# Optimization experiments

Hardware: AMD Instinct MI355X
Metric: run time of the kernel (lower is better)

Reference implementation:

```python
import jax, jax.numpy as jnp
import numpy as np

COMMITMENT_COST = 1.0


def setup_inputs() -> dict:
    key = jax.random.key(0)
    k1, k2 = jax.random.split(key)
    x = jax.random.normal(k1, (8, 4096, 256), dtype=jnp.float32)
    codebook = jax.random.normal(k2, (2048, 256), dtype=jnp.float32)
    return {"x": x, "codebook": codebook}


def reference(x, codebook):
    # Squared Euclidean distances via the GEMM expansion:
    # argmin over torch.cdist (sqrt is monotone); dist values are unused.
    x2 = jnp.sum(x * x, axis=-1, keepdims=True)            # [B, T, 1]
    c2 = jnp.sum(codebook * codebook, axis=-1)             # [N]
    d2 = x2 - 2.0 * jnp.einsum('btd,nd->btn', x, codebook) + c2  # [B, T, N]
    indices = jnp.argmin(d2, axis=-1)                      # [B, T]
    codes = codebook[indices]                              # [B, T, D]

    code_loss = jnp.mean((codes - jax.lax.stop_gradient(x)) ** 2)
    embedding_loss = jnp.mean((x - jax.lax.stop_gradient(codes)) ** 2) * COMMITMENT_COST
    loss = code_loss + embedding_loss

    # Straight-through estimator
    quantized = x + jax.lax.stop_gradient(codes - x)
    return quantized, indices, loss
```

## Files before the change

### kernel.cpp

```cpp
#include <hip/hip_runtime.h>

#define D   256
#define BM  64
#define BN  128
#define KC  64

typedef __attribute__((ext_vector_type(8))) short v8s;
typedef __attribute__((ext_vector_type(4))) float v4f;
#define MFMA16 __builtin_amdgcn_mfma_f32_16x16x32_bf16

#define WAITVM(N) asm volatile("s_waitcnt vmcnt(" #N ")" ::: "memory")

static __device__ inline unsigned short f2bf(float f) {
    unsigned u = __float_as_uint(f);
    return (unsigned short)((u + 0x7fffu + ((u >> 16) & 1u)) >> 16);
}
static __device__ inline float bf2f(unsigned short s) {
    return __uint_as_float(((unsigned)s) << 16);
}

static __device__ inline void gl_lds16(const unsigned short* g, unsigned short* l) {
    __builtin_amdgcn_global_load_lds(
        (const __attribute__((address_space(1))) unsigned int*)g,
        (__attribute__((address_space(3))) unsigned int*)l, 16, 0, 0);
}

__global__ void vq_prep_sw(const float* __restrict__ cb,
                           unsigned short* __restrict__ cbh, unsigned short* __restrict__ cbl,
                           float* __restrict__ c2) {
    const int chunk = blockIdx.x;
    const int nc = (chunk >> 2) * BN;
    const int kc = (chunk & 3) * KC;
    #pragma unroll
    for (int i = 0; i < 4; ++i) {
        const int p   = i * 256 + threadIdx.x;
        const int seg = p >> 7;
        const int n   = (p & 127) ^ seg;
        const float* src = cb + (size_t)(nc + n) * D + kc + seg * 8;
        const float4 f0 = *reinterpret_cast<const float4*>(src);
        const float4 f1 = *reinterpret_cast<const float4*>(src + 4);
        const float f[8] = {f0.x, f0.y, f0.z, f0.w, f1.x, f1.y, f1.z, f1.w};
        v8s h, l;
        #pragma unroll
        for (int j = 0; j < 8; ++j) {
            unsigned short hb = f2bf(f[j]);
            h[j] = (short)hb;
            l[j] = (short)f2bf(f[j] - bf2f(hb));
        }
        const size_t o = ((size_t)chunk * 1024 + p) * 8;
        *reinterpret_cast<v8s*>(cbh + o) = h;
        *reinterpret_cast<v8s*>(cbl + o) = l;
    }
    if ((chunk & 3) == 0) {
        const int w    = threadIdx.x >> 6;
        const int lane = threadIdx.x & 63;
        for (int r = w; r < BN; r += 4) {
            const float4 v = *reinterpret_cast<const float4*>(cb + (size_t)(nc + r) * D + lane * 4);
            float s = v.x * v.x + v.y * v.y + v.z * v.z + v.w * v.w;
            #pragma unroll
            for (int off = 32; off > 0; off >>= 1) s += __shfl_down(s, off, 64);
            if (lane == 0) c2[nc + r] = s;
        }
    }
}

__global__ __launch_bounds__(256, 2) void vq_argmin_mfma(
        const float* __restrict__ x, const float* __restrict__ cb,
        const unsigned short* __restrict__ cbh, const unsigned short* __restrict__ cbl,
        const float* __restrict__ c2, float* __restrict__ idx_out,
        float* __restrict__ qout, float* __restrict__ partial, int N) {
    __shared__ unsigned short lds_h[2][BN * 8 * 8];
    __shared__ unsigned short lds_l[2][BN * 8 * 8];
    __shared__ float red_v[64 * 32];
    __shared__ int   red_i[64 * 32];

    const int tid  = threadIdx.x;
    const int w    = tid >> 6;
    const int lane = tid & 63;
    const int col  = lane & 15;
    const int quad = lane >> 4;
    const int mg   = w >> 1;
    const int ng   = w & 1;
    const int m0   = blockIdx.x * BM;
    const int n_groups = N >> 7;
    const int n_stages = n_groups * 4;

    const unsigned short* gh0 = cbh + ((size_t)(w * 256 + lane)) * 8;
    const unsigned short* gl0 = cbl + ((size_t)(w * 256 + lane)) * 8;

    #pragma unroll
    for (int i = 0; i < 4; ++i) {
        gl_lds16(gh0 + i * 512, &lds_h[0][(w * 256 + i * 64) * 8]);
        gl_lds16(gl0 + i * 512, &lds_l[0][(w * 256 + i * 64) * 8]);
    }

    v8s xh[2][8], xl[2][8];
    #pragma unroll
    for (int mt = 0; mt < 2; ++mt) {
        const float* xr = x + (size_t)(m0 + mg * 32 + mt * 16 + col) * D;
        #pragma unroll
        for (int ks = 0; ks < 8; ++ks) {
            const int kb = ks * 32 + quad * 8;
            const float4 f0 = *reinterpret_cast<const float4*>(xr + kb);
            const float4 f1 = *reinterpret_cast<const float4*>(xr + kb + 4);
            float f[8] = {f0.x, f0.y, f0.z, f0.w, f1.x, f1.y, f1.z, f1.w};
            v8s h, l;
            #pragma unroll
            for (int j = 0; j < 8; ++j) {
                unsigned short hb = f2bf(f[j]);
                h[j] = (short)hb;
                l[j] = (short)f2bf(f[j] - bf2f(hb));
            }
            xh[mt][ks] = h; xl[mt][ks] = l;
        }
    }

    float runmin[2][4];
    int   runidx[2][4];
    #pragma unroll
    for (int mt = 0; mt < 2; ++mt)
        #pragma unroll
        for (int r = 0; r < 4; ++r) { runmin[mt][r] = 3.4e38f; runidx[mt][r] = 0; }

    v4f acc[4][2];
    #pragma unroll
    for (int nt = 0; nt < 4; ++nt)
        #pragma unroll
        for (int mt = 0; mt < 2; ++mt) acc[nt][mt] = 0.0f;

    for (int g = 0; g < n_groups; ++g) {
        float c2f[4];
        #pragma unroll
        for (int nt = 0; nt < 4; ++nt) c2f[nt] = c2[g * BN + ng * 64 + nt * 16 + col];

        #pragma unroll
        for (int cc = 0; cc < 4; ++cc) {
            const int par   = cc & 1;
            const int stage = g * 4 + cc;
            const bool more = (stage + 1 < n_stages);

            WAITVM(4);
            __builtin_amdgcn_s_barrier();
            if (more) {
                const unsigned short* gh = gh0 + (size_t)(stage + 1) * 8192;
                unsigned short* lh = lds_h[par ^ 1];
                #pragma unroll
                for (int i = 0; i < 4; ++i) gl_lds16(gh + i * 512, lh + (w * 256 + i * 64) * 8);
            }
            __builtin_amdgcn_s_setprio(1);
            #pragma unroll
            for (int ksk = 0; ksk < 2; ++ksk) {
                const int ks  = cc * 2 + ksk;
                const int seg = ksk * 4 + quad;
                #pragma unroll
                for (int nt = 0; nt < 4; ++nt) {
                    const int p = seg * BN + ((ng * 64 + nt * 16 + col) ^ seg);
                    const v8s ch = *reinterpret_cast<const v8s*>(&lds_h[par][p * 8]);
                    #pragma unroll
                    for (int mt = 0; mt < 2; ++mt) {
                        acc[nt][mt] = MFMA16(xh[mt][ks], ch, acc[nt][mt], 0, 0, 0);
                        acc[nt][mt] = MFMA16(xl[mt][ks], ch, acc[nt][mt], 0, 0, 0);
                    }
                }
            }
            __builtin_amdgcn_s_setprio(0);

            if (more) { WAITVM(4); }
            else      { WAITVM(0); }
            __builtin_amdgcn_s_barrier();
            if (more) {
                const unsigned short* gl = gl0 + (size_t)(stage + 1) * 8192;
                unsigned short* ll = lds_l[par ^ 1];
                #pragma unroll
                for (int i = 0; i < 4; ++i) gl_lds16(gl + i * 512, ll + (w * 256 + i * 64) * 8);
            }
            __builtin_amdgcn_s_setprio(1);
            #pragma unroll
            for (int ksk = 0; ksk < 2; ++ksk) {
                const int ks  = cc * 2 + ksk;
                const int seg = ksk * 4 + quad;
                #pragma unroll
                for (int nt = 0; nt < 4; ++nt) {
                    const int p = seg * BN + ((ng * 64 + nt * 16 + col) ^ seg);
                    const v8s cl = *reinterpret_cast<const v8s*>(&lds_l[par][p * 8]);
                    #pragma unroll
                    for (int mt = 0; mt < 2; ++mt)
                        acc[nt][mt] = MFMA16(xh[mt][ks], cl, acc[nt][mt], 0, 0, 0);
                }
            }
            __builtin_amdgcn_s_setprio(0);
        }

        const int nc = g * BN;
        #pragma unroll
        for (int nt = 0; nt < 4; ++nt) {
            const int n = nc + ng * 64 + nt * 16 + col;
            #pragma unroll
            for (int mt = 0; mt < 2; ++mt) {
                #pragma unroll
                for (int r = 0; r < 4; ++r) {
                    const float s = c2f[nt] - 2.0f * acc[nt][mt][r];
                    if (s < runmin[mt][r]) { runmin[mt][r] = s; runidx[mt][r] = n; }
                }
                acc[nt][mt] = 0.0f;
            }
        }
    }

    __syncthreads();
    #pragma unroll
    for (int mt = 0; mt < 2; ++mt)
        #pragma unroll
        for (int r = 0; r < 4; ++r) {
            const int row  = mg * 32 + mt * 16 + quad * 4 + r;
            const int slot = (ng * 16 + col) ^ (row & 31);
            red_v[row * 32 + slot] = runmin[mt][r];
            red_i[row * 32 + slot] = runidx[mt][r];
        }
    __syncthreads();
    float best = 3.4e38f;
    int   bidx = 0;
    if (tid < 64) {
        #pragma unroll 4
        for (int t = 0; t < 32; ++t) {
            const int  sl = t ^ (tid & 31);
            const float v = red_v[tid * 32 + sl];
            const int  id = red_i[tid * 32 + sl];
            if (v < best || (v == best && id < bidx)) { best = v; bidx = id; }
        }
        idx_out[m0 + tid] = (float)bidx;
    }
    __syncthreads();
    int* idx_sh = reinterpret_cast<int*>(red_v);
    if (tid < 64) idx_sh[tid] = bidx;
    __syncthreads();

    const float* xg2 = x + (size_t)m0 * D;
    float s = 0.0f;
    #pragma unroll
    for (int i = 0; i < 16; ++i) {
        const int g   = i * 256 + tid;
        const int row = g >> 6;
        const int k4  = (g & 63) * 4;
        const int idx = idx_sh[row];
        const float4 c  = *reinterpret_cast<const float4*>(cb  + (size_t)idx * D + k4);
        const float4 xv = *reinterpret_cast<const float4*>(xg2 + (size_t)row * D + k4);
        *reinterpret_cast<float4*>(qout + (size_t)(m0 + row) * D + k4) = c;
        const float dx = c.x - xv.x, dy = c.y - xv.y, dz = c.z - xv.z, dw = c.w - xv.w;
        s += dx * dx + dy * dy + dz * dz + dw * dw;
    }
    #pragma unroll
    for (int off = 32; off > 0; off >>= 1) s += __shfl_down(s, off, 64);
    float* wsum = reinterpret_cast<float*>(red_i);
    if ((tid & 63) == 0) wsum[tid >> 6] = s;
    __syncthreads();
    if (tid == 0) partial[blockIdx.x] = wsum[0] + wsum[1] + wsum[2] + wsum[3];
}

__global__ void vq_reduce_kernel(const float* __restrict__ partial, float* __restrict__ loss,
                                 float scale, int n) {
    __shared__ float red[4];
    const int tid = threadIdx.x;
    float s = 0.0f;
    for (int i = tid; i < n; i += 256) s += partial[i];
    #pragma unroll
    for (int off = 32; off > 0; off >>= 1) s += __shfl_down(s, off, 64);
    if ((tid & 63) == 0) red[tid >> 6] = s;
    __syncthreads();
    if (tid == 0) loss[0] = (red[0] + red[1] + red[2] + red[3]) * scale;
}

extern "C" void kernel_launch(void* const* d_in, const int* in_sizes, int n_in,
                              void* d_out, int out_size, void* d_ws, size_t ws_size,
                              hipStream_t stream) {
    const float* x  = (const float*)d_in[0];
    const float* cb = (const float*)d_in[1];
    const int M = in_sizes[0] / D;
    const int N = in_sizes[1] / D;

    float* qout    = (float*)d_out;
    float* idx_out = qout + (size_t)M * D;
    float* loss    = idx_out + M;

    char* wsb = (char*)d_ws;
    float*          c2      = (float*)wsb;
    unsigned short* cbh     = (unsigned short*)(wsb + 8192);
    unsigned short* cbl     = cbh + (size_t)N * D;
    float*          partial = (float*)(wsb + 8192 + 2 * (size_t)N * D * sizeof(unsigned short));

    vq_prep_sw<<<(N / BN) * (D / KC), 256, 0, stream>>>(cb, cbh, cbl, c2);
    vq_argmin_mfma<<<M / BM, 256, 0, stream>>>(x, cb, cbh, cbl, c2, idx_out, qout, partial, N);
    const float scale = 2.0f / (float)((size_t)M * D);
    vq_reduce_kernel<<<1, 256, 0, stream>>>(partial, loss, scale, M / BM);
}
```

Before: 204.6 us.

## Double row tile to 128 with 512 threads, stage c2 in LDS, atomic loss

```diff
diff --git a/kernel.cpp b/kernel.cpp
--- a/kernel.cpp
+++ b/kernel.cpp
@@ -1,15 +1,15 @@
 #include <hip/hip_runtime.h>
 
 #define D   256
-#define BM  64
+#define BM  128
 #define BN  128
-#define KC  64
 
 typedef __attribute__((ext_vector_type(8))) short v8s;
 typedef __attribute__((ext_vector_type(4))) float v4f;
 #define MFMA16 __builtin_amdgcn_mfma_f32_16x16x32_bf16
 
 #define WAITVM(N) asm volatile("s_waitcnt vmcnt(" #N ")" ::: "memory")
+#define SCHEDFENCE() __builtin_amdgcn_sched_barrier(0)
 
 static __device__ inline unsigned short f2bf(float f) {
     unsigned u = __float_as_uint(f);
@@ -25,54 +25,51 @@
         (__attribute__((address_space(3))) unsigned int*)l, 16, 0, 0);
 }
 
+__global__ void vq_prep_c2(const float* __restrict__ cb, float* __restrict__ c2,
+                           float* __restrict__ loss) {
+    const int row  = blockIdx.x;
+    const int lane = threadIdx.x;
+    if (row == 0 && lane == 0) loss[0] = 0.0f;
+    const float4 v = *reinterpret_cast<const float4*>(cb + (size_t)row * D + lane * 4);
+    float s = v.x * v.x + v.y * v.y + v.z * v.z + v.w * v.w;
+    #pragma unroll
+    for (int off = 32; off > 0; off >>= 1) s += __shfl_down(s, off, 64);
+    if (lane == 0) c2[row] = s;
+}
+
 __global__ void vq_prep_sw(const float* __restrict__ cb,
-                           unsigned short* __restrict__ cbh, unsigned short* __restrict__ cbl,
-                           float* __restrict__ c2) {
-    const int chunk = blockIdx.x;
+                           unsigned short* __restrict__ cbh, unsigned short* __restrict__ cbl) {
+    const int b     = blockIdx.x;
+    const int chunk = b >> 2;
     const int nc = (chunk >> 2) * BN;
-    const int kc = (chunk & 3) * KC;
-    #pragma unroll
-    for (int i = 0; i < 4; ++i) {
-        const int p   = i * 256 + threadIdx.x;
-        const int seg = p >> 7;
-        const int n   = (p & 127) ^ seg;
-        const float* src = cb + (size_t)(nc + n) * D + kc + seg * 8;
-        const float4 f0 = *reinterpret_cast<const float4*>(src);
-        const float4 f1 = *reinterpret_cast<const float4*>(src + 4);
-        const float f[8] = {f0.x, f0.y, f0.z, f0.w, f1.x, f1.y, f1.z, f1.w};
-        v8s h, l;
-        #pragma unroll
-        for (int j = 0; j < 8; ++j) {
-            unsigned short hb = f2bf(f[j]);
-            h[j] = (short)hb;
-            l[j] = (short)f2bf(f[j] - bf2f(hb));
-        }
-        const size_t o = ((size_t)chunk * 1024 + p) * 8;
-        *reinterpret_cast<v8s*>(cbh + o) = h;
-        *reinterpret_cast<v8s*>(cbl + o) = l;
-    }
-    if ((chunk & 3) == 0) {
-        const int w    = threadIdx.x >> 6;
-        const int lane = threadIdx.x & 63;
-        for (int r = w; r < BN; r += 4) {
-            const float4 v = *reinterpret_cast<const float4*>(cb + (size_t)(nc + r) * D + lane * 4);
-            float s = v.x * v.x + v.y * v.y + v.z * v.z + v.w * v.w;
-            #pragma unroll
-            for (int off = 32; off > 0; off >>= 1) s += __shfl_down(s, off, 64);
-            if (lane == 0) c2[nc + r] = s;
-        }
-    }
-}
-
-__global__ __launch_bounds__(256, 2) void vq_argmin_mfma(
+    const int kc = (chunk & 3) * 64;
+    const int p   = (b & 3) * 256 + threadIdx.x;
+    const int seg = p >> 7;
+    const int n   = (p & 127) ^ seg;
+    const float* src = cb + (size_t)(nc + n) * D + kc + seg * 8;
+    const float4 f0 = *reinterpret_cast<const float4*>(src);
+    const float4 f1 = *reinterpret_cast<const float4*>(src + 4);
+    const float f[8] = {f0.x, f0.y, f0.z, f0.w, f1.x, f1.y, f1.z, f1.w};
+    v8s h, l;
+    #pragma unroll
+    for (int j = 0; j < 8; ++j) {
+        unsigned short hb = f2bf(f[j]);
+        h[j] = (short)hb;
+        l[j] = (short)f2bf(f[j] - bf2f(hb));
+    }
+    const size_t o = ((size_t)chunk * 1024 + p) * 8;
+    *reinterpret_cast<v8s*>(cbh + o) = h;
+    *reinterpret_cast<v8s*>(cbl + o) = l;
+}
+
+__global__ __launch_bounds__(512, 2) void vq_argmin_mfma(
         const float* __restrict__ x, const float* __restrict__ cb,
         const unsigned short* __restrict__ cbh, const unsigned short* __restrict__ cbl,
         const float* __restrict__ c2, float* __restrict__ idx_out,
-        float* __restrict__ qout, float* __restrict__ partial, int N) {
-    __shared__ unsigned short lds_h[2][BN * 8 * 8];
-    __shared__ unsigned short lds_l[2][BN * 8 * 8];
-    __shared__ float red_v[64 * 32];
-    __shared__ int   red_i[64 * 32];
+        float* __restrict__ qout, float* __restrict__ loss, float scale, int N) {
+    __shared__ unsigned short lds_h[2][8192];
+    __shared__ unsigned short lds_l[2][8192];
+    __shared__ float c2s[2048];
 
     const int tid  = threadIdx.x;
     const int w    = tid >> 6;
@@ -85,13 +82,22 @@
     const int n_groups = N >> 7;
     const int n_stages = n_groups * 4;
 
-    const unsigned short* gh0 = cbh + ((size_t)(w * 256 + lane)) * 8;
-    const unsigned short* gl0 = cbl + ((size_t)(w * 256 + lane)) * 8;
-
-    #pragma unroll
-    for (int i = 0; i < 4; ++i) {
-        gl_lds16(gh0 + i * 512, &lds_h[0][(w * 256 + i * 64) * 8]);
-        gl_lds16(gl0 + i * 512, &lds_l[0][(w * 256 + i * 64) * 8]);
+    const unsigned short* gh0 = cbh + ((size_t)(w * 128 + lane)) * 8;
+    const unsigned short* gl0 = cbl + ((size_t)(w * 128 + lane)) * 8;
+
+    gl_lds16(gh0,       &lds_h[0][w * 1024]);
+    gl_lds16(gh0 + 512, &lds_h[0][w * 1024 + 512]);
+    gl_lds16(gl0,       &lds_l[0][w * 1024]);
+    gl_lds16(gl0 + 512, &lds_l[0][w * 1024 + 512]);
+
+    {
+        const int o = tid * 8;
+        if (o < N) {
+            const float4 a = *reinterpret_cast<const float4*>(c2 + o);
+            const float4 b = *reinterpret_cast<const float4*>(c2 + o + 4);
+            *reinterpret_cast<float4*>(&c2s[o])     = a;
+            *reinterpret_cast<float4*>(&c2s[o + 4]) = b;
+        }
     }
 
     v8s xh[2][8], xl[2][8];
@@ -128,24 +134,24 @@
         #pragma unroll
         for (int mt = 0; mt < 2; ++mt) acc[nt][mt] = 0.0f;
 
+    __syncthreads();
+
     for (int g = 0; g < n_groups; ++g) {
-        float c2f[4];
-        #pragma unroll
-        for (int nt = 0; nt < 4; ++nt) c2f[nt] = c2[g * BN + ng * 64 + nt * 16 + col];
-
         #pragma unroll
         for (int cc = 0; cc < 4; ++cc) {
             const int par   = cc & 1;
             const int stage = g * 4 + cc;
             const bool more = (stage + 1 < n_stages);
 
-            WAITVM(4);
+            WAITVM(2);
+            SCHEDFENCE();
             __builtin_amdgcn_s_barrier();
+            SCHEDFENCE();
             if (more) {
                 const unsigned short* gh = gh0 + (size_t)(stage + 1) * 8192;
-                unsigned short* lh = lds_h[par ^ 1];
-                #pragma unroll
-                for (int i = 0; i < 4; ++i) gl_lds16(gh + i * 512, lh + (w * 256 + i * 64) * 8);
+                unsigned short* lh = &lds_h[par ^ 1][w * 1024];
+                gl_lds16(gh,       lh);
+                gl_lds16(gh + 512, lh + 512);
             }
             __builtin_amdgcn_s_setprio(1);
             #pragma unroll
@@ -165,14 +171,16 @@
             }
             __builtin_amdgcn_s_setprio(0);
 
-            if (more) { WAITVM(4); }
+            if (more) { WAITVM(2); }
             else      { WAITVM(0); }
+            SCHEDFENCE();
             __builtin_amdgcn_s_barrier();
+            SCHEDFENCE();
             if (more) {
                 const unsigned short* gl = gl0 + (size_t)(stage + 1) * 8192;
-                unsigned short* ll = lds_l[par ^ 1];
-                #pragma unroll
-                for (int i = 0; i < 4; ++i) gl_lds16(gl + i * 512, ll + (w * 256 + i * 64) * 8);
+                unsigned short* ll = &lds_l[par ^ 1][w * 1024];
+                gl_lds16(gl,       ll);
+                gl_lds16(gl + 512, ll + 512);
             }
             __builtin_amdgcn_s_setprio(1);
             #pragma unroll
@@ -191,15 +199,15 @@
             __builtin_amdgcn_s_setprio(0);
         }
 
-        const int nc = g * BN;
         #pragma unroll
         for (int nt = 0; nt < 4; ++nt) {
-            const int n = nc + ng * 64 + nt * 16 + col;
+            const int n = g * BN + ng * 64 + nt * 16 + col;
+            const float c2n = c2s[n];
             #pragma unroll
             for (int mt = 0; mt < 2; ++mt) {
                 #pragma unroll
                 for (int r = 0; r < 4; ++r) {
-                    const float s = c2f[nt] - 2.0f * acc[nt][mt][r];
+                    const float s = c2n - 2.0f * acc[nt][mt][r];
                     if (s < runmin[mt][r]) { runmin[mt][r] = s; runidx[mt][r] = n; }
                 }
                 acc[nt][mt] = 0.0f;
@@ -208,6 +216,8 @@
     }
 
     __syncthreads();
+    float* red_v = reinterpret_cast<float*>(&lds_h[0][0]);
+    int*   red_i = reinterpret_cast<int*>(&lds_l[0][0]);
     #pragma unroll
     for (int mt = 0; mt < 2; ++mt)
         #pragma unroll
@@ -220,7 +230,7 @@
     __syncthreads();
     float best = 3.4e38f;
     int   bidx = 0;
-    if (tid < 64) {
+    if (tid < 128) {
         #pragma unroll 4
         for (int t = 0; t < 32; ++t) {
             const int  sl = t ^ (tid & 31);
@@ -231,17 +241,17 @@
         idx_out[m0 + tid] = (float)bidx;
     }
     __syncthreads();
-    int* idx_sh = reinterpret_cast<int*>(red_v);
-    if (tid < 64) idx_sh[tid] = bidx;
+    int* idx_sh = reinterpret_cast<int*>(&lds_h[1][0]);
+    if (tid < 128) idx_sh[tid] = bidx;
     __syncthreads();
 
     const float* xg2 = x + (size_t)m0 * D;
     float s = 0.0f;
     #pragma unroll
     for (int i = 0; i < 16; ++i) {
-        const int g   = i * 256 + tid;
-        const int row = g >> 6;
-        const int k4  = (g & 63) * 4;
+        const int gix = i * 512 + tid;
+        const int row = gix >> 6;
+        const int k4  = (gix & 63) * 4;
         const int idx = idx_sh[row];
         const float4 c  = *reinterpret_cast<const float4*>(cb  + (size_t)idx * D + k4);
         const float4 xv = *reinterpret_cast<const float4*>(xg2 + (size_t)row * D + k4);
@@ -251,23 +261,15 @@
     }
     #pragma unroll
     for (int off = 32; off > 0; off >>= 1) s += __shfl_down(s, off, 64);
-    float* wsum = reinterpret_cast<float*>(red_i);
+    float* wsum = reinterpret_cast<float*>(&lds_l[1][0]);
     if ((tid & 63) == 0) wsum[tid >> 6] = s;
     __syncthreads();
-    if (tid == 0) partial[blockIdx.x] = wsum[0] + wsum[1] + wsum[2] + wsum[3];
-}
-
-__global__ void vq_reduce_kernel(const float* __restrict__ partial, float* __restrict__ loss,
-                                 float scale, int n) {
-    __shared__ float red[4];
-    const int tid = threadIdx.x;
-    float s = 0.0f;
-    for (int i = tid; i < n; i += 256) s += partial[i];
-    #pragma unroll
-    for (int off = 32; off > 0; off >>= 1) s += __shfl_down(s, off, 64);
-    if ((tid & 63) == 0) red[tid >> 6] = s;
-    __syncthreads();
-    if (tid == 0) loss[0] = (red[0] + red[1] + red[2] + red[3]) * scale;
+    if (tid == 0) {
+        float t = 0.0f;
+        #pragma unroll
+        for (int i = 0; i < 8; ++i) t += wsum[i];
+        atomicAdd(loss, t * scale);
+    }
 }
 
 extern "C" void kernel_launch(void* const* d_in, const int* in_sizes, int n_in,
@@ -283,13 +285,13 @@
     float* loss    = idx_out + M;
 
     char* wsb = (char*)d_ws;
-    float*          c2      = (float*)wsb;
-    unsigned short* cbh     = (unsigned short*)(wsb + 8192);
-    unsigned short* cbl     = cbh + (size_t)N * D;
-    float*          partial = (float*)(wsb + 8192 + 2 * (size_t)N * D * sizeof(unsigned short));
-
-    vq_prep_sw<<<(N / BN) * (D / KC), 256, 0, stream>>>(cb, cbh, cbl, c2);
-    vq_argmin_mfma<<<M / BM, 256, 0, stream>>>(x, cb, cbh, cbl, c2, idx_out, qout, partial, N);
+    float*          c2  = (float*)wsb;
+    unsigned short* cbh = (unsigned short*)(wsb + 8192);
+    unsigned short* cbl = cbh + (size_t)N * D;
+
+    vq_prep_c2<<<N, 64, 0, stream>>>(cb, c2, loss);
+    vq_prep_sw<<<(N / BN) * 4 * 4, 256, 0, stream>>>(cb, cbh, cbl);
     const float scale = 2.0f / (float)((size_t)M * D);
-    vq_reduce_kernel<<<1, 256, 0, stream>>>(partial, loss, scale, M / BM);
-}
+    vq_argmin_mfma<<<M / BM, 512, 0, stream>>>(x, cb, cbh, cbl, c2, idx_out, qout,
+                                               loss, scale, N);
+}
```

Result: slower. 223.7 us (+9.3%).
